# Kernel tuning notes

Hardware: AMD Instinct MI355X
Metric: run time of the kernel (lower is better)

## Reference

```python
import jax, jax.numpy as jnp
import numpy as np

N = 100000      # nodes
E = 1600000     # edges (before self loops)
H = 64          # hidden channels (per-head out dim, concat=False)
HEADS = 2
L = 2           # num GAT blocks
IN = 64
OUT = 10
B = 64          # graphs in batch
SLOPE = 0.2     # LeakyReLU negative slope (GATv2Conv default)
EPS = 1e-5      # BatchNorm eps


def setup_inputs() -> dict:
    key = jax.random.key(0)
    ks = jax.random.split(key, 10)
    s = 0.05
    x = jax.random.normal(ks[0], (N, IN), jnp.float32)
    edge_index = jax.random.randint(ks[1], (2, E), 0, N, dtype=jnp.int64)
    batch = jnp.sort(jax.random.randint(ks[2], (N,), 0, B, dtype=jnp.int64))
    W_enc = jax.random.normal(ks[3], (IN, H), jnp.float32) * s
    b_enc = jnp.zeros((H,), jnp.float32)
    Wl = jax.random.normal(ks[4], (L, H, HEADS * H), jnp.float32) * s
    bl = jnp.zeros((L, HEADS * H), jnp.float32)
    Wr = jax.random.normal(ks[5], (L, H, HEADS * H), jnp.float32) * s
    br = jnp.zeros((L, HEADS * H), jnp.float32)
    att = jax.random.normal(ks[6], (L, HEADS, H), jnp.float32) * s
    bias = jnp.zeros((L, H), jnp.float32)
    gamma = jnp.ones((L, H), jnp.float32)
    beta = jnp.zeros((L, H), jnp.float32)
    W_cls = jax.random.normal(ks[7], (H, OUT), jnp.float32) * s
    b_cls = jnp.zeros((OUT,), jnp.float32)
    return dict(x=x, edge_index=edge_index, batch=batch, W_enc=W_enc, b_enc=b_enc,
                Wl=Wl, bl=bl, Wr=Wr, br=br, att=att, bias=bias,
                gamma=gamma, beta=beta, W_cls=W_cls, b_cls=b_cls)


def reference(x, edge_index, batch, W_enc, b_enc, Wl, bl, Wr, br, att, bias,
              gamma, beta, W_cls, b_cls):
    # add self loops (GATv2Conv default add_self_loops=True)
    loops = jnp.arange(N, dtype=edge_index.dtype)
    ei = jnp.concatenate([edge_index, jnp.stack([loops, loops])], axis=1)
    src, dst = ei[0], ei[1]

    h = x @ W_enc + b_enc                                   # [N, H] atom encoder (Linear)
    for l in range(L):
        xl = (h @ Wl[l] + bl[l]).reshape(N, HEADS, H)       # source transform
        xr = (h @ Wr[l] + br[l]).reshape(N, HEADS, H)       # target transform
        # GATv2: e_uv = a^T LeakyReLU(W_l x_u + W_r x_v)
        z = jax.nn.leaky_relu(xl[src] + xr[dst], SLOPE)     # [E', heads, H]
        e = jnp.einsum('ehc,hc->eh', z, att[l])             # [E', heads]
        # segment softmax over incoming edges of each dst node
        m = jax.ops.segment_max(e, dst, num_segments=N)     # [N, heads]
        ex = jnp.exp(e - m[dst])
        den = jax.ops.segment_sum(ex, dst, num_segments=N)
        alpha = ex / den[dst]                               # [E', heads]
        out = jax.ops.segment_sum(xl[src] * alpha[:, :, None], dst, num_segments=N)
        h_new = out.mean(axis=1) + bias[l]                  # concat=False: mean over heads
        # BatchNorm1d (batch statistics) -> ReLU; dropout=0
        mu = h_new.mean(axis=0)
        var = h_new.var(axis=0)
        h = jax.nn.relu((h_new - mu) * jax.lax.rsqrt(var + EPS) * gamma[l] + beta[l])

    # global mean pool over graphs
    cnt = jax.ops.segment_sum(jnp.ones((N,), h.dtype), batch, num_segments=B)
    g = jax.ops.segment_sum(h, batch, num_segments=B) / jnp.maximum(cnt, 1.0)[:, None]
    return g @ W_cls + b_cls                                # [B, OUT]
```

## Files before the change

### kernel.cpp

```cpp
#include <hip/hip_runtime.h>

#define N_NODES 100000
#define E_EDGES 1600000
#define EP_EDGES (E_EDGES + N_NODES)
#define SLOPE 0.2f
#define BN_EPS 1e-5f
#define NB 8
#define NODES_PER_B 12500
#define NREP 32
#define SUBREG 8192
#define SCATTER_BLKS ((EP_EDGES + 255) / 256)

typedef _Float16 h2 __attribute__((ext_vector_type(2)));

#if defined(__has_builtin)
#if __has_builtin(__builtin_amdgcn_fdot2)
#define HAVE_FDOT2 1
#endif
#endif

__device__ __forceinline__ float fdot2f(h2 a, h2 b, float c) {
#ifdef HAVE_FDOT2
    return __builtin_amdgcn_fdot2(a, b, c, false);
#else
    return c + (float)a[0] * (float)b[0] + (float)a[1] * (float)b[1];
#endif
}
__device__ __forceinline__ h2 bch2(unsigned u) { return __builtin_bit_cast(h2, u); }
__device__ __forceinline__ h2 habs2(h2 z) {
    return __builtin_bit_cast(h2, (unsigned)(__builtin_bit_cast(unsigned, z) & 0x7fff7fffu));
}
__device__ __forceinline__ h2 shflx_h2(h2 a, int o) {
    return __builtin_bit_cast(h2, __shfl_xor(__builtin_bit_cast(int, a), o, 64));
}

template <int CTRL>
__device__ __forceinline__ float dpp_add_step(float v) {
    int r = __builtin_amdgcn_update_dpp(0, __float_as_int(v), CTRL, 0xF, 0xF, false);
    return v + __int_as_float(r);
}
__device__ __forceinline__ float rowsum16(float v) {
    v = dpp_add_step<0x128>(v);
    v = dpp_add_step<0x124>(v);
    v = dpp_add_step<0x122>(v);
    v = dpp_add_step<0x121>(v);
    return v;
}

__device__ __forceinline__ void bucket_scatter_body(int bid, const int* __restrict__ src,
                                                    const int* __restrict__ dst,
                                                    int* __restrict__ gcur, unsigned* __restrict__ ebuf) {
    int i = bid * 256 + threadIdx.x;
    int rep = bid & (NREP - 1);
    bool active = i < EP_EDGES;
    int s = 0, d = 0;
    if (i < E_EDGES) { s = src[i]; d = dst[i]; }
    else if (active) { s = i - E_EDGES; d = s; }
    int b = active ? (int)((unsigned)d / NODES_PER_B) : NB;
    unsigned long long lt = (1ull << (threadIdx.x & 63)) - 1ull;
    int rank = 0;
    unsigned long long mymask = 0;
#pragma unroll
    for (int bb = 0; bb < NB; ++bb) {
        unsigned long long m = __ballot(b == bb);
        if (b == bb) { rank = __popcll(m & lt); mymask = m; }
    }
    int leader = mymask ? (__ffsll((long long)mymask) - 1) : 0;
    int lanebit = threadIdx.x & 63;
    int chunkbase = 0;
    if (active && lanebit == leader)
        chunkbase = atomicAdd(&gcur[rep * NB + b], (int)__popcll(mymask));
    chunkbase = __shfl(chunkbase, leader, 64);
    if (active) {
        unsigned dl = (unsigned)d - (unsigned)b * NODES_PER_B;
        ebuf[(size_t)(rep * NB + b) * SUBREG + chunkbase + rank] = (dl << 17) | (unsigned)s;
    }
}

__device__ __forceinline__ void fuse_enc_body(const float* __restrict__ We, const float* __restrict__ be,
                                              const float* __restrict__ Wl, const float* __restrict__ bl,
                                              const float* __restrict__ Wr, const float* __restrict__ br,
                                              float* __restrict__ Wcl, float* __restrict__ bcl,
                                              float* __restrict__ Wcr, float* __restrict__ bcr,
                                              float (*sWe)[64], float* sbe) {
    int t = threadIdx.x;
    for (int i = t; i < 4096; i += 256) sWe[i & 63][i >> 6] = We[i];
    if (t < 64) sbe[t] = be[t];
    __syncthreads();
    int j = t & 127, side = t >> 7;
    const float* W  = side ? Wr : Wl;
    const float* bb = side ? br : bl;
    float acc[64];
#pragma unroll
    for (int k = 0; k < 64; ++k) acc[k] = 0.f;
    float bacc = bb[j];
    for (int m = 0; m < 64; ++m) {
        float wv = W[m * 128 + j];
        bacc += sbe[m] * wv;
#pragma unroll
        for (int k = 0; k < 64; ++k) acc[k] += sWe[m][k] * wv;
    }
    float* Wc = side ? Wcr : Wcl;
#pragma unroll
    for (int k = 0; k < 64; ++k) Wc[k * 128 + j] = acc[k];
    (side ? bcr : bcl)[j] = bacc;
}

__global__ __launch_bounds__(256) void scatter_fuse(const int* __restrict__ src, const int* __restrict__ dst,
                                                    int* __restrict__ gcur, unsigned* __restrict__ ebuf,
                                                    const float* __restrict__ We, const float* __restrict__ be,
                                                    const float* __restrict__ Wl, const float* __restrict__ bl,
                                                    const float* __restrict__ Wr, const float* __restrict__ br,
                                                    float* __restrict__ Wcl, float* __restrict__ bcl,
                                                    float* __restrict__ Wcr, float* __restrict__ bcr) {
    __shared__ float sWe[64][64];
    __shared__ float sbe[64];
    if (blockIdx.x == 0)
        fuse_enc_body(We, be, Wl, bl, Wr, br, Wcl, bcl, Wcr, bcr, sWe, sbe);
    else
        bucket_scatter_body(blockIdx.x - 1, src, dst, gcur, ebuf);
}

template <int BN>
__device__ __forceinline__ void layer_gemm_body(int bid, int nb,
                                                const float* __restrict__ hin,
                                                const float* __restrict__ Wl, const float* __restrict__ bl,
                                                const float* __restrict__ Wr, const float* __restrict__ br,
                                                const float* __restrict__ bns, const float* __restrict__ gamma,
                                                const float* __restrict__ beta,
                                                unsigned short* __restrict__ xl, unsigned short* __restrict__ xr,
                                                float* ssc, float* ssh, h2 (*sh)[36]) {
    int t = threadIdx.x;
    if (BN) {
        if (t < 64) {
            float s = 0.f, sq = 0.f;
#pragma unroll
            for (int r = 0; r < 8; ++r) { s += bns[r * 128 + t]; sq += bns[r * 128 + 64 + t]; }
            float mu = s * (1.f / N_NODES);
            float var = sq * (1.f / N_NODES) - mu * mu;
            float sc = gamma[t] * rsqrtf(var + BN_EPS);
            ssc[t] = sc; ssh[t] = beta[t] - mu * sc;
        }
        __syncthreads();
    }
    int p = t & 127, rh = t >> 7;
    int col0 = 2 * p;
    bool isR = col0 >= 128;
    int cw0 = col0 & 127, cw1 = cw0 + 1;
    const float* W = isR ? Wr : Wl;
    h2 w2a[32], w2b[32];
#pragma unroll
    for (int k2 = 0; k2 < 32; ++k2) {
        w2a[k2] = (h2){(_Float16)W[(2 * k2) * 128 + cw0], (_Float16)W[(2 * k2 + 1) * 128 + cw0]};
        w2b[k2] = (h2){(_Float16)W[(2 * k2) * 128 + cw1], (_Float16)W[(2 * k2 + 1) * 128 + cw1]};
    }
    float bja = (isR ? br : bl)[cw0];
    float bjb = (isR ? br : bl)[cw1];
    int head0 = cw0 >> 6, c0 = cw0 & 63;
    int head1 = cw1 >> 6, c1 = cw1 & 63;
    int oidx0 = ((c0 >> 2) << 3) + (head0 << 2) + (c0 & 3);
    int oidx1 = ((c1 >> 2) << 3) + (head1 << 2) + (c1 & 3);
    unsigned short* dstp = isR ? xr : xl;
    for (int base = bid * 16; base < N_NODES; base += nb * 16) {
        __syncthreads();
#pragma unroll
        for (int pass = 0; pass < 2; ++pass) {
            int i = t + pass * 256;
            int node = i >> 5, pr = i & 31;
            int gnode = base + node;
            int cc = pr * 2;
            float2 v = make_float2(0.f, 0.f);
            if (gnode < N_NODES) v = *(const float2*)(hin + (size_t)gnode * 64 + cc);
            if (BN) {
                v.x = fmaxf(v.x * ssc[cc] + ssh[cc], 0.f);
                v.y = fmaxf(v.y * ssc[cc + 1] + ssh[cc + 1], 0.f);
            }
            sh[node][pr] = (h2){(_Float16)v.x, (_Float16)v.y};
        }
        __syncthreads();
        int lim = min(16, N_NODES - base);
        int rend = min(rh * 8 + 8, lim);
        for (int r = rh * 8; r < rend; ++r) {
            float acca = bja, accb = bjb;
            const uint4* r4 = (const uint4*)(&sh[r][0]);
#pragma unroll
            for (int k4 = 0; k4 < 8; ++k4) {
                uint4 u = r4[k4];
                acca = fdot2f(bch2(u.x), w2a[4 * k4 + 0], acca);
                accb = fdot2f(bch2(u.x), w2b[4 * k4 + 0], accb);
                acca = fdot2f(bch2(u.y), w2a[4 * k4 + 1], acca);
                accb = fdot2f(bch2(u.y), w2b[4 * k4 + 1], accb);
                acca = fdot2f(bch2(u.z), w2a[4 * k4 + 2], acca);
                accb = fdot2f(bch2(u.z), w2b[4 * k4 + 2], accb);
                acca = fdot2f(bch2(u.w), w2a[4 * k4 + 3], acca);
                accb = fdot2f(bch2(u.w), w2b[4 * k4 + 3], accb);
            }
            size_t rowb = (size_t)(base + r) * 128;
            dstp[rowb + oidx0] = __builtin_bit_cast(unsigned short, (_Float16)acca);
            dstp[rowb + oidx1] = __builtin_bit_cast(unsigned short, (_Float16)accb);
        }
    }
}

__global__ __launch_bounds__(256) void deg_gemm0(const int* __restrict__ gcur,
                                                 const unsigned* __restrict__ ebuf,
                                                 int* __restrict__ deg,
                                                 const float* __restrict__ hin,
                                                 const float* __restrict__ Wl, const float* __restrict__ bl,
                                                 const float* __restrict__ Wr, const float* __restrict__ br,
                                                 unsigned short* __restrict__ xl, unsigned short* __restrict__ xr) {
    __shared__ unsigned ldeg2[NODES_PER_B / 2];
    __shared__ float ssc[64], ssh[64];
    __shared__ h2 sh[16][36];
    if (blockIdx.x < NREP * NB) {
        int b = blockIdx.x & (NB - 1), rep = blockIdx.x >> 3;
        for (int j = threadIdx.x; j < NODES_PER_B / 2; j += 256) ldeg2[j] = 0;
        __syncthreads();
        int cnt = gcur[rep * NB + b];
        int base = b * NODES_PER_B;
        const unsigned* p = ebuf + (size_t)(rep * NB + b) * SUBREG;
        for (int i = threadIdx.x; i < cnt; i += 256) {
            unsigned dl = p[i] >> 17;
            atomicAdd(&ldeg2[dl >> 1], 1u << ((dl & 1) * 16));
        }
        __syncthreads();
        for (int j = threadIdx.x; j < NODES_PER_B; j += 256) {
            unsigned v = (ldeg2[j >> 1] >> ((j & 1) * 16)) & 0xffffu;
            if (v) atomicAdd(&deg[base + j], (int)v);
        }
    } else {
        layer_gemm_body<0>(blockIdx.x - NREP * NB, 1024, hin, Wl, bl, Wr, br,
                           nullptr, nullptr, nullptr, xl, xr, ssc, ssh, sh);
    }
}

__global__ __launch_bounds__(256) void bucket_fine(const int* __restrict__ gcur,
                                                   const unsigned* __restrict__ ebuf,
                                                   int* __restrict__ cursor, int* __restrict__ col) {
    int b = blockIdx.x & (NB - 1), rep = blockIdx.x >> 3;
    int cnt = gcur[rep * NB + b];
    int base = b * NODES_PER_B;
    const unsigned* p = ebuf + (size_t)(rep * NB + b) * SUBREG;
    for (int i = threadIdx.x; i < cnt; i += 256) {
        unsigned e = p[i];
        int d = base + (int)(e >> 17), s = (int)(e & 0x1FFFFu);
        int pos = atomicAdd(&cursor[d], 1);
        col[pos] = s;
    }
}

__global__ void scan_a(const int* __restrict__ deg, int* __restrict__ row_ptr, int* __restrict__ bsum) {
    __shared__ int wsum[16];
    int tid = threadIdx.x;
    int lane = tid & 63;
    int i = blockIdx.x * 1024 + tid;
    int x = (i < N_NODES) ? deg[i] : 0;
#pragma unroll
    for (int o = 1; o < 64; o <<= 1) {
        int y = __shfl_up(x, o, 64);
        if (lane >= o) x += y;
    }
    if (lane == 63) wsum[tid >> 6] = x;
    __syncthreads();
    if (tid < 16) {
        int s = wsum[tid];
#pragma unroll
        for (int o = 1; o < 16; o <<= 1) {
            int y = __shfl_up(s, o, 16);
            if (tid >= o) s += y;
        }
        wsum[tid] = s;
    }
    __syncthreads();
    int pre = (tid >= 64) ? wsum[(tid >> 6) - 1] : 0;
    int incl = x + pre;
    if (i < N_NODES) row_ptr[i + 1] = incl;
    if (tid == 1023) bsum[blockIdx.x] = incl;
}

__global__ void scan_c(int* __restrict__ cursor, int* __restrict__ row_ptr, const int* __restrict__ bsum) {
    __shared__ int sp[128];
    int t = threadIdx.x;
    if (t < 128) sp[t] = (t < 98) ? bsum[t] : 0;
    __syncthreads();
    for (int o = 1; o < 128; o <<= 1) {
        int v = (t < 128 && t >= o) ? sp[t - o] : 0;
        __syncthreads();
        if (t < 128) sp[t] += v;
        __syncthreads();
    }
    int i = blockIdx.x * 256 + t;
    if (i < N_NODES) {
        int d = cursor[i];
        int blk = i >> 10;
        int pre = blk ? sp[blk - 1] : 0;
        int incl = row_ptr[i + 1] + pre;
        row_ptr[i + 1] = incl;
        cursor[i] = incl - d;
        if (i == 0) row_ptr[0] = 0;
    }
}

__global__ __launch_bounds__(256) void layer_gemm1(const float* __restrict__ hin,
                                                   const float* __restrict__ Wl, const float* __restrict__ bl,
                                                   const float* __restrict__ Wr, const float* __restrict__ br,
                                                   const float* __restrict__ bns, const float* __restrict__ gamma,
                                                   const float* __restrict__ beta,
                                                   unsigned short* __restrict__ xl, unsigned short* __restrict__ xr) {
    __shared__ float ssc[64], ssh[64];
    __shared__ h2 sh[16][36];
    layer_gemm_body<1>(blockIdx.x, gridDim.x, hin, Wl, bl, Wr, br, bns, gamma, beta, xl, xr, ssc, ssh, sh);
}

__global__ __launch_bounds__(256) void aggregate(const char* __restrict__ xlb,
                                                 const uint4* __restrict__ xr4,
                                                 const int* __restrict__ row_ptr, const int* __restrict__ col,
                                                 const float* __restrict__ att_l, const float* __restrict__ bias_l,
                                                 float* __restrict__ hn, float* __restrict__ bnsum) {
    int lane = threadIdx.x & 63, wid = threadIdx.x >> 6;
    int q = lane >> 4, k = lane & 15;
    int koff = k << 4;
    h2 atA0 = {(_Float16)att_l[4 * k], (_Float16)att_l[4 * k + 1]};
    h2 atA1 = {(_Float16)att_l[4 * k + 2], (_Float16)att_l[4 * k + 3]};
    h2 atB0 = {(_Float16)att_l[64 + 4 * k], (_Float16)att_l[64 + 4 * k + 1]};
    h2 atB1 = {(_Float16)att_l[64 + 4 * k + 2], (_Float16)att_l[64 + 4 * k + 3]};
    float bi0 = bias_l[4 * k], bi1 = bias_l[4 * k + 1], bi2 = bias_l[4 * k + 2], bi3 = bias_l[4 * k + 3];
    const h2 c06 = {(_Float16)0.6f, (_Float16)0.6f};
    const h2 c04 = {(_Float16)0.4f, (_Float16)0.4f};
    float ps[4] = {0, 0, 0, 0}, pq[4] = {0, 0, 0, 0};
    int w = blockIdx.x * 4 + wid, nw = gridDim.x * 4;
    for (int v = w; v < N_NODES; v += nw) {
        uint4 rp = xr4[(size_t)v * 16 + k];
        h2 rA0 = bch2(rp.x), rA1 = bch2(rp.y), rB0 = bch2(rp.z), rB1 = bch2(rp.w);
        int beg = row_ptr[v], end = row_ptr[v + 1];
        float s0 = 0.f, s1 = 0.f;
        h2 aA0 = {0, 0}, aA1 = {0, 0}, aB0 = {0, 0}, aB1 = {0, 0};
        const int* cptr = col + beg + q;
        int cv0 = cptr[0], cv1 = cptr[4], cv2 = cptr[8], cv3 = cptr[12];
        cptr += 16;
        uint4 lp0 = *(const uint4*)(xlb + (((size_t)(unsigned)cv0) << 8) + koff);
        uint4 lp1 = lp0, lp2 = lp0;
        if (beg + 4 < end) lp1 = *(const uint4*)(xlb + (((size_t)(unsigned)cv1) << 8) + koff);
        if (beg + 8 < end) lp2 = *(const uint4*)(xlb + (((size_t)(unsigned)cv2) << 8) + koff);
#pragma unroll 2
        for (int i = beg; i < end; i += 4) {
            uint4 lp3 = lp2;
            if (i + 12 < end) lp3 = *(const uint4*)(xlb + (((size_t)(unsigned)cv3) << 8) + koff);
            cv3 = *cptr; cptr += 4;
            h2 lA0 = bch2(lp0.x), lA1 = bch2(lp0.y), lB0 = bch2(lp0.z), lB1 = bch2(lp0.w);
            h2 zA0 = lA0 + rA0, zA1 = lA1 + rA1, zB0 = lB0 + rB0, zB1 = lB1 + rB1;
            h2 yA0 = zA0 * c06 + habs2(zA0) * c04;
            h2 yA1 = zA1 * c06 + habs2(zA1) * c04;
            h2 yB0 = zB0 * c06 + habs2(zB0) * c04;
            h2 yB1 = zB1 * c06 + habs2(zB1) * c04;
            float t0 = fdot2f(yA1, atA1, fdot2f(yA0, atA0, 0.f));
            float t1 = fdot2f(yB1, atB1, fdot2f(yB0, atB0, 0.f));
            t0 = rowsum16(t0); t1 = rowsum16(t1);
            bool valid = (i + q) < end;
            float p0 = valid ? __expf(t0) : 0.f;
            float p1 = valid ? __expf(t1) : 0.f;
            s0 += p0; s1 += p1;
            h2 p0h = {(_Float16)p0, (_Float16)p0};
            h2 p1h = {(_Float16)p1, (_Float16)p1};
            aA0 += p0h * lA0; aA1 += p0h * lA1;
            aB0 += p1h * lB0; aB1 += p1h * lB1;
            lp0 = lp1; lp1 = lp2; lp2 = lp3;
        }
#pragma unroll
        for (int o = 16; o <= 32; o <<= 1) {
            s0 += __shfl_xor(s0, o, 64); s1 += __shfl_xor(s1, o, 64);
            aA0 += shflx_h2(aA0, o); aA1 += shflx_h2(aA1, o);
            aB0 += shflx_h2(aB0, o); aB1 += shflx_h2(aB1, o);
        }
        if (q == 0) {
            float i0 = 0.5f / s0, i1 = 0.5f / s1;
            float hv0 = (float)aA0[0] * i0 + (float)aB0[0] * i1 + bi0;
            float hv1 = (float)aA0[1] * i0 + (float)aB0[1] * i1 + bi1;
            float hv2 = (float)aA1[0] * i0 + (float)aB1[0] * i1 + bi2;
            float hv3 = (float)aA1[1] * i0 + (float)aB1[1] * i1 + bi3;
            *(float4*)(hn + (size_t)v * 64 + 4 * k) = make_float4(hv0, hv1, hv2, hv3);
            ps[0] += hv0; pq[0] += hv0 * hv0;
            ps[1] += hv1; pq[1] += hv1 * hv1;
            ps[2] += hv2; pq[2] += hv2 * hv2;
            ps[3] += hv3; pq[3] += hv3 * hv3;
        }
    }
    __shared__ float sb[2][4][64];
    if (q == 0) {
#pragma unroll
        for (int j = 0; j < 4; ++j) { sb[0][wid][4 * k + j] = ps[j]; sb[1][wid][4 * k + j] = pq[j]; }
    }
    __syncthreads();
    float* dstb = bnsum + (size_t)(blockIdx.x & 7) * 128;
    int t = threadIdx.x;
    if (t < 64)
        atomicAdd(&dstb[t], sb[0][0][t] + sb[0][1][t] + sb[0][2][t] + sb[0][3][t]);
    else if (t < 128)
        atomicAdd(&dstb[t], sb[1][0][t - 64] + sb[1][1][t - 64] + sb[1][2][t - 64] + sb[1][3][t - 64]);
}

__global__ __launch_bounds__(256) void pool2(const float* __restrict__ hn, const int* __restrict__ batch,
                                             const float* __restrict__ bns, const float* __restrict__ gamma,
                                             const float* __restrict__ beta,
                                             float* __restrict__ gpool, float* __restrict__ gcnt) {
    __shared__ float ssc[64], ssh[64];
    int t = threadIdx.x;
    if (t < 64) {
        float s = 0.f, sq = 0.f;
#pragma unroll
        for (int r = 0; r < 8; ++r) { s += bns[r * 128 + t]; sq += bns[r * 128 + 64 + t]; }
        float mu = s * (1.f / N_NODES);
        float var = sq * (1.f / N_NODES) - mu * mu;
        float sc = gamma[t] * rsqrtf(var + BN_EPS);
        ssc[t] = sc; ssh[t] = beta[t] - mu * sc;
    }
    __syncthreads();
    int g = blockIdx.x >> 2, part = blockIdx.x & 3;
    int lo = 0, hi = N_NODES;
    while (lo < hi) { int mid = (lo + hi) >> 1; if (batch[mid] < g) lo = mid + 1; else hi = mid; }
    int lo2 = lo, hi2 = N_NODES;
    while (lo2 < hi2) { int mid = (lo2 + hi2) >> 1; if (batch[mid] < g + 1) lo2 = mid + 1; else hi2 = mid; }
    int len = lo2 - lo;
    if (part == 0 && t == 0) gcnt[g] = (float)len;
    int n0 = lo + (len * part) / 4, n1 = lo + (len * (part + 1)) / 4;
    int c = t & 63, r = t >> 6;
    float sc = ssc[c], sh = ssh[c];
    float acc = 0.f;
    for (int node = n0 + r; node < n1; node += 4)
        acc += fmaxf(hn[(size_t)node * 64 + c] * sc + sh, 0.f);
    __shared__ float sb[4][64];
    sb[r][c] = acc;
    __syncthreads();
    if (r == 0)
        atomicAdd(&gpool[g * 64 + c], sb[0][c] + sb[1][c] + sb[2][c] + sb[3][c]);
}

__global__ void classify(const float* __restrict__ gpool, const float* __restrict__ gcnt,
                         const float* __restrict__ Wc, const float* __restrict__ bc, float* __restrict__ out) {
    int t = threadIdx.x;
    if (t >= 640) return;
    int b = t / 10, o = t % 10;
    float inv = 1.f / fmaxf(gcnt[b], 1.f);
    float acc = 0.f;
    for (int c = 0; c < 64; ++c) acc += gpool[b * 64 + c] * Wc[c * 10 + o];
    out[t] = acc * inv + bc[o];
}

extern "C" void kernel_launch(void* const* d_in, const int* in_sizes, int n_in,
                              void* d_out, int out_size, void* d_ws, size_t ws_size,
                              hipStream_t stream) {
    (void)in_sizes; (void)n_in; (void)out_size; (void)ws_size;
    const float* x     = (const float*)d_in[0];
    const int*   ei    = (const int*)d_in[1];
    const int*   batch = (const int*)d_in[2];
    const float* W_enc = (const float*)d_in[3];
    const float* b_enc = (const float*)d_in[4];
    const float* Wl    = (const float*)d_in[5];
    const float* bl    = (const float*)d_in[6];
    const float* Wr    = (const float*)d_in[7];
    const float* br    = (const float*)d_in[8];
    const float* att   = (const float*)d_in[9];
    const float* bias  = (const float*)d_in[10];
    const float* gamma = (const float*)d_in[11];
    const float* beta  = (const float*)d_in[12];
    const float* Wc    = (const float*)d_in[13];
    const float* bc    = (const float*)d_in[14];
    float* out = (float*)d_out;

    char* ws = (char*)d_ws;
    size_t off = 0;
    auto A = [&](size_t bytes) { size_t r = off; off += (bytes + 255) & ~(size_t)255; return r; };

    int* row_ptr = (int*)(ws + A((N_NODES + 1) * 4));
    size_t colv_off = A((size_t)EP_EDGES * 4 + 426240);
    int* colv = (int*)(ws + colv_off);
    char* zbase = ws + colv_off + (size_t)EP_EDGES * 4;
    int*   cursor = (int*)(zbase + 128);
    int*   gcur   = (int*)(zbase + 400128);
    float* bns    = (float*)(zbase + 401152);
    float* gpool  = (float*)(zbase + 409344);
    float* gcnt   = (float*)(zbase + 425728);
    const size_t ZBYTES = 426240;

    float* h   = (float*)(ws + A((size_t)N_NODES * 64 * 4));
    float* hn  = (float*)(ws + A((size_t)N_NODES * 64 * 4));
    unsigned short* xl = (unsigned short*)(ws + A((size_t)N_NODES * 128 * 2));
    unsigned short* xr = (unsigned short*)(ws + A((size_t)N_NODES * 128 * 2));
    unsigned* ebuf = (unsigned*)(ws + A((size_t)NREP * NB * SUBREG * 4));
    int* bsum  = (int*)(ws + A(512));
    float* Wcl = (float*)(ws + A(64 * 128 * 4));
    float* Wcr = (float*)(ws + A(64 * 128 * 4));
    float* bcl = (float*)(ws + A(128 * 4));
    float* bcr = (float*)(ws + A(128 * 4));

    const int* srcv = ei;
    const int* dstv = ei + E_EDGES;

    hipMemsetAsync(zbase, 0, ZBYTES, stream);

    scatter_fuse<<<SCATTER_BLKS + 1, 256, 0, stream>>>(srcv, dstv, gcur, ebuf,
                                                       W_enc, b_enc, Wl, bl, Wr, br,
                                                       Wcl, bcl, Wcr, bcr);
    deg_gemm0<<<NREP * NB + 1024, 256, 0, stream>>>(gcur, ebuf, cursor,
                                                    x, Wcl, bcl, Wcr, bcr, xl, xr);
    scan_a<<<98, 1024, 0, stream>>>(cursor, row_ptr, bsum);
    scan_c<<<(N_NODES + 255) / 256, 256, 0, stream>>>(cursor, row_ptr, bsum);
    bucket_fine<<<NREP * NB, 256, 0, stream>>>(gcur, ebuf, cursor, colv);

    aggregate<<<4096, 256, 0, stream>>>((const char*)xl, (const uint4*)xr,
                                        row_ptr, colv, att, bias, hn, bns);
    layer_gemm1<<<1024, 256, 0, stream>>>(hn, Wl + 64 * 128, bl + 128, Wr + 64 * 128, br + 128,
                                          bns, gamma, beta, xl, xr);
    aggregate<<<4096, 256, 0, stream>>>((const char*)xl, (const uint4*)xr,
                                        row_ptr, colv, att + 128, bias + 64, h, bns + 1024);

    pool2<<<256, 256, 0, stream>>>(h, batch, bns + 1024, gamma + 64, beta + 64, gpool, gcnt);
    classify<<<1, 640, 0, stream>>>(gpool, gcnt, Wc, bc, out);
}
```

Measured before the change: 432.5 us.

## Store hidden states in fp16, fold slope into attention, fuse classifier into pool

The aggregate output now goes to a half-precision buffer instead of fp32, which halves the traffic for the layer GEMM and pool reads. The LeakyReLU constants are folded into pre-scaled attention vectors, so per-edge multiplies become extra dot2 ops. The classifier is merged into the pool kernel through a last-block atomic counter, saving one launch. The degree histogram packs four 8-bit counters per word. That narrowing risks overflow if any node gets more than 255 in-edges in one sub-bucket, and the fp16 activations lose some accuracy.

```diff
diff --git a/kernel.cpp b/kernel.cpp
--- a/kernel.cpp
+++ b/kernel.cpp
@@ -27,6 +27,7 @@
 #endif
 }
 __device__ __forceinline__ h2 bch2(unsigned u) { return __builtin_bit_cast(h2, u); }
+__device__ __forceinline__ unsigned bcu(h2 v) { return __builtin_bit_cast(unsigned, v); }
 __device__ __forceinline__ h2 habs2(h2 z) {
     return __builtin_bit_cast(h2, (unsigned)(__builtin_bit_cast(unsigned, z) & 0x7fff7fffu));
 }
@@ -123,7 +124,7 @@
 
 template <int BN>
 __device__ __forceinline__ void layer_gemm_body(int bid, int nb,
-                                                const float* __restrict__ hin,
+                                                const void* __restrict__ hin,
                                                 const float* __restrict__ Wl, const float* __restrict__ bl,
                                                 const float* __restrict__ Wr, const float* __restrict__ br,
                                                 const float* __restrict__ bns, const float* __restrict__ gamma,
@@ -169,13 +170,17 @@
             int node = i >> 5, pr = i & 31;
             int gnode = base + node;
             int cc = pr * 2;
-            float2 v = make_float2(0.f, 0.f);
-            if (gnode < N_NODES) v = *(const float2*)(hin + (size_t)gnode * 64 + cc);
             if (BN) {
-                v.x = fmaxf(v.x * ssc[cc] + ssh[cc], 0.f);
-                v.y = fmaxf(v.y * ssc[cc + 1] + ssh[cc + 1], 0.f);
+                unsigned u = (gnode < N_NODES) ? ((const unsigned*)hin)[(size_t)gnode * 32 + pr] : 0u;
+                h2 hv = bch2(u);
+                float vx = fmaxf((float)hv[0] * ssc[cc] + ssh[cc], 0.f);
+                float vy = fmaxf((float)hv[1] * ssc[cc + 1] + ssh[cc + 1], 0.f);
+                sh[node][pr] = (h2){(_Float16)vx, (_Float16)vy};
+            } else {
+                float2 v = make_float2(0.f, 0.f);
+                if (gnode < N_NODES) v = *(const float2*)((const float*)hin + (size_t)gnode * 64 + cc);
+                sh[node][pr] = (h2){(_Float16)v.x, (_Float16)v.y};
             }
-            sh[node][pr] = (h2){(_Float16)v.x, (_Float16)v.y};
         }
         __syncthreads();
         int lim = min(16, N_NODES - base);
@@ -209,23 +214,23 @@
                                                  const float* __restrict__ Wl, const float* __restrict__ bl,
                                                  const float* __restrict__ Wr, const float* __restrict__ br,
                                                  unsigned short* __restrict__ xl, unsigned short* __restrict__ xr) {
-    __shared__ unsigned ldeg2[NODES_PER_B / 2];
+    __shared__ unsigned ldeg4[NODES_PER_B / 4 + 1];
     __shared__ float ssc[64], ssh[64];
     __shared__ h2 sh[16][36];
     if (blockIdx.x < NREP * NB) {
         int b = blockIdx.x & (NB - 1), rep = blockIdx.x >> 3;
-        for (int j = threadIdx.x; j < NODES_PER_B / 2; j += 256) ldeg2[j] = 0;
+        for (int j = threadIdx.x; j < NODES_PER_B / 4 + 1; j += 256) ldeg4[j] = 0;
         __syncthreads();
         int cnt = gcur[rep * NB + b];
         int base = b * NODES_PER_B;
         const unsigned* p = ebuf + (size_t)(rep * NB + b) * SUBREG;
         for (int i = threadIdx.x; i < cnt; i += 256) {
             unsigned dl = p[i] >> 17;
-            atomicAdd(&ldeg2[dl >> 1], 1u << ((dl & 1) * 16));
+            atomicAdd(&ldeg4[dl >> 2], 1u << ((dl & 3) * 8));
         }
         __syncthreads();
         for (int j = threadIdx.x; j < NODES_PER_B; j += 256) {
-            unsigned v = (ldeg2[j >> 1] >> ((j & 1) * 16)) & 0xffffu;
+            unsigned v = (ldeg4[j >> 2] >> ((j & 3) * 8)) & 0xffu;
             if (v) atomicAdd(&deg[base + j], (int)v);
         }
     } else {
@@ -301,7 +306,7 @@
     }
 }
 
-__global__ __launch_bounds__(256) void layer_gemm1(const float* __restrict__ hin,
+__global__ __launch_bounds__(256) void layer_gemm1(const unsigned short* __restrict__ hin,
                                                    const float* __restrict__ Wl, const float* __restrict__ bl,
                                                    const float* __restrict__ Wr, const float* __restrict__ br,
                                                    const float* __restrict__ bns, const float* __restrict__ gamma,
@@ -316,17 +321,19 @@
                                                  const uint4* __restrict__ xr4,
                                                  const int* __restrict__ row_ptr, const int* __restrict__ col,
                                                  const float* __restrict__ att_l, const float* __restrict__ bias_l,
-                                                 float* __restrict__ hn, float* __restrict__ bnsum) {
+                                                 unsigned short* __restrict__ hn16, float* __restrict__ bnsum) {
     int lane = threadIdx.x & 63, wid = threadIdx.x >> 6;
     int q = lane >> 4, k = lane & 15;
     int koff = k << 4;
-    h2 atA0 = {(_Float16)att_l[4 * k], (_Float16)att_l[4 * k + 1]};
-    h2 atA1 = {(_Float16)att_l[4 * k + 2], (_Float16)att_l[4 * k + 3]};
-    h2 atB0 = {(_Float16)att_l[64 + 4 * k], (_Float16)att_l[64 + 4 * k + 1]};
-    h2 atB1 = {(_Float16)att_l[64 + 4 * k + 2], (_Float16)att_l[64 + 4 * k + 3]};
+    h2 a6A0 = {(_Float16)(0.6f * att_l[4 * k]), (_Float16)(0.6f * att_l[4 * k + 1])};
+    h2 a6A1 = {(_Float16)(0.6f * att_l[4 * k + 2]), (_Float16)(0.6f * att_l[4 * k + 3])};
+    h2 a4A0 = {(_Float16)(0.4f * att_l[4 * k]), (_Float16)(0.4f * att_l[4 * k + 1])};
+    h2 a4A1 = {(_Float16)(0.4f * att_l[4 * k + 2]), (_Float16)(0.4f * att_l[4 * k + 3])};
+    h2 a6B0 = {(_Float16)(0.6f * att_l[64 + 4 * k]), (_Float16)(0.6f * att_l[64 + 4 * k + 1])};
+    h2 a6B1 = {(_Float16)(0.6f * att_l[64 + 4 * k + 2]), (_Float16)(0.6f * att_l[64 + 4 * k + 3])};
+    h2 a4B0 = {(_Float16)(0.4f * att_l[64 + 4 * k]), (_Float16)(0.4f * att_l[64 + 4 * k + 1])};
+    h2 a4B1 = {(_Float16)(0.4f * att_l[64 + 4 * k + 2]), (_Float16)(0.4f * att_l[64 + 4 * k + 3])};
     float bi0 = bias_l[4 * k], bi1 = bias_l[4 * k + 1], bi2 = bias_l[4 * k + 2], bi3 = bias_l[4 * k + 3];
-    const h2 c06 = {(_Float16)0.6f, (_Float16)0.6f};
-    const h2 c04 = {(_Float16)0.4f, (_Float16)0.4f};
     float ps[4] = {0, 0, 0, 0}, pq[4] = {0, 0, 0, 0};
     int w = blockIdx.x * 4 + wid, nw = gridDim.x * 4;
     for (int v = w; v < N_NODES; v += nw) {
@@ -349,12 +356,10 @@
             cv3 = *cptr; cptr += 4;
             h2 lA0 = bch2(lp0.x), lA1 = bch2(lp0.y), lB0 = bch2(lp0.z), lB1 = bch2(lp0.w);
             h2 zA0 = lA0 + rA0, zA1 = lA1 + rA1, zB0 = lB0 + rB0, zB1 = lB1 + rB1;
-            h2 yA0 = zA0 * c06 + habs2(zA0) * c04;
-            h2 yA1 = zA1 * c06 + habs2(zA1) * c04;
-            h2 yB0 = zB0 * c06 + habs2(zB0) * c04;
-            h2 yB1 = zB1 * c06 + habs2(zB1) * c04;
-            float t0 = fdot2f(yA1, atA1, fdot2f(yA0, atA0, 0.f));
-            float t1 = fdot2f(yB1, atB1, fdot2f(yB0, atB0, 0.f));
+            float t0 = fdot2f(habs2(zA1), a4A1, fdot2f(habs2(zA0), a4A0,
+                       fdot2f(zA1, a6A1, fdot2f(zA0, a6A0, 0.f))));
+            float t1 = fdot2f(habs2(zB1), a4B1, fdot2f(habs2(zB0), a4B0,
+                       fdot2f(zB1, a6B1, fdot2f(zB0, a6B0, 0.f))));
             t0 = rowsum16(t0); t1 = rowsum16(t1);
             bool valid = (i + q) < end;
             float p0 = valid ? __expf(t0) : 0.f;
@@ -378,7 +383,9 @@
             float hv1 = (float)aA0[1] * i0 + (float)aB0[1] * i1 + bi1;
             float hv2 = (float)aA1[0] * i0 + (float)aB1[0] * i1 + bi2;
             float hv3 = (float)aA1[1] * i0 + (float)aB1[1] * i1 + bi3;
-            *(float4*)(hn + (size_t)v * 64 + 4 * k) = make_float4(hv0, hv1, hv2, hv3);
+            h2 o01 = {(_Float16)hv0, (_Float16)hv1};
+            h2 o23 = {(_Float16)hv2, (_Float16)hv3};
+            *(uint2*)(hn16 + (size_t)v * 64 + 4 * k) = make_uint2(bcu(o01), bcu(o23));
             ps[0] += hv0; pq[0] += hv0 * hv0;
             ps[1] += hv1; pq[1] += hv1 * hv1;
             ps[2] += hv2; pq[2] += hv2 * hv2;
@@ -399,11 +406,15 @@
         atomicAdd(&dstb[t], sb[1][0][t - 64] + sb[1][1][t - 64] + sb[1][2][t - 64] + sb[1][3][t - 64]);
 }
 
-__global__ __launch_bounds__(256) void pool2(const float* __restrict__ hn, const int* __restrict__ batch,
-                                             const float* __restrict__ bns, const float* __restrict__ gamma,
-                                             const float* __restrict__ beta,
-                                             float* __restrict__ gpool, float* __restrict__ gcnt) {
+__global__ __launch_bounds__(256) void pool_cls(const unsigned short* __restrict__ hn,
+                                                const int* __restrict__ batch,
+                                                const float* __restrict__ bns, const float* __restrict__ gamma,
+                                                const float* __restrict__ beta,
+                                                const float* __restrict__ Wc, const float* __restrict__ bcb,
+                                                float* __restrict__ gpool, float* __restrict__ gcnt,
+                                                int* __restrict__ pcount, float* __restrict__ out) {
     __shared__ float ssc[64], ssh[64];
+    __shared__ int lastf;
     int t = threadIdx.x;
     if (t < 64) {
         float s = 0.f, sq = 0.f;
@@ -426,24 +437,29 @@
     int c = t & 63, r = t >> 6;
     float sc = ssc[c], sh = ssh[c];
     float acc = 0.f;
-    for (int node = n0 + r; node < n1; node += 4)
-        acc += fmaxf(hn[(size_t)node * 64 + c] * sc + sh, 0.f);
+    for (int node = n0 + r; node < n1; node += 4) {
+        float hv = (float)__builtin_bit_cast(_Float16, hn[(size_t)node * 64 + c]);
+        acc += fmaxf(hv * sc + sh, 0.f);
+    }
     __shared__ float sb[4][64];
     sb[r][c] = acc;
     __syncthreads();
     if (r == 0)
         atomicAdd(&gpool[g * 64 + c], sb[0][c] + sb[1][c] + sb[2][c] + sb[3][c]);
-}
-
-__global__ void classify(const float* __restrict__ gpool, const float* __restrict__ gcnt,
-                         const float* __restrict__ Wc, const float* __restrict__ bc, float* __restrict__ out) {
-    int t = threadIdx.x;
-    if (t >= 640) return;
-    int b = t / 10, o = t % 10;
-    float inv = 1.f / fmaxf(gcnt[b], 1.f);
-    float acc = 0.f;
-    for (int c = 0; c < 64; ++c) acc += gpool[b * 64 + c] * Wc[c * 10 + o];
-    out[t] = acc * inv + bc[o];
+    __threadfence();
+    __syncthreads();
+    if (t == 0) lastf = (atomicAdd(pcount, 1) == (int)gridDim.x - 1);
+    __syncthreads();
+    if (lastf) {
+        __threadfence();
+        for (int i = t; i < 640; i += 256) {
+            int b = i / 10, o = i % 10;
+            float inv = 1.f / fmaxf(gcnt[b], 1.f);
+            float a = 0.f;
+            for (int cc = 0; cc < 64; ++cc) a += gpool[b * 64 + cc] * Wc[cc * 10 + o];
+            out[i] = a * inv + bcb[o];
+        }
+    }
 }
 
 extern "C" void kernel_launch(void* const* d_in, const int* in_sizes, int n_in,
@@ -472,7 +488,7 @@
     auto A = [&](size_t bytes) { size_t r = off; off += (bytes + 255) & ~(size_t)255; return r; };
 
     int* row_ptr = (int*)(ws + A((N_NODES + 1) * 4));
-    size_t colv_off = A((size_t)EP_EDGES * 4 + 426240);
+    size_t colv_off = A((size_t)EP_EDGES * 4 + 426496);
     int* colv = (int*)(ws + colv_off);
     char* zbase = ws + colv_off + (size_t)EP_EDGES * 4;
     int*   cursor = (int*)(zbase + 128);
@@ -480,10 +496,11 @@
     float* bns    = (float*)(zbase + 401152);
     float* gpool  = (float*)(zbase + 409344);
     float* gcnt   = (float*)(zbase + 425728);
-    const size_t ZBYTES = 426240;
-
-    float* h   = (float*)(ws + A((size_t)N_NODES * 64 * 4));
-    float* hn  = (float*)(ws + A((size_t)N_NODES * 64 * 4));
+    int*   pcount = (int*)(zbase + 425984);
+    const size_t ZBYTES = 426496;
+
+    unsigned short* hn = (unsigned short*)(ws + A((size_t)N_NODES * 64 * 2));
+    unsigned short* h2buf = (unsigned short*)(ws + A((size_t)N_NODES * 64 * 2));
     unsigned short* xl = (unsigned short*)(ws + A((size_t)N_NODES * 128 * 2));
     unsigned short* xr = (unsigned short*)(ws + A((size_t)N_NODES * 128 * 2));
     unsigned* ebuf = (unsigned*)(ws + A((size_t)NREP * NB * SUBREG * 4));
@@ -512,8 +529,8 @@
     layer_gemm1<<<1024, 256, 0, stream>>>(hn, Wl + 64 * 128, bl + 128, Wr + 64 * 128, br + 128,
                                           bns, gamma, beta, xl, xr);
     aggregate<<<4096, 256, 0, stream>>>((const char*)xl, (const uint4*)xr,
-                                        row_ptr, colv, att + 128, bias + 64, h, bns + 1024);
-
-    pool2<<<256, 256, 0, stream>>>(h, batch, bns + 1024, gamma + 64, beta + 64, gpool, gcnt);
-    classify<<<1, 640, 0, stream>>>(gpool, gcnt, Wc, bc, out);
-}
+                                        row_ptr, colv, att + 128, bias + 64, h2buf, bns + 1024);
+
+    pool_cls<<<256, 256, 0, stream>>>(h2buf, batch, bns + 1024, gamma + 64, beta + 64,
+                                      Wc, bc, gpool, gcnt, pcount, out);
+}
```

After: 452.7 us. 4.7% more time.
